# Performance work log

Hardware: AMD Instinct MI355X
Metric: run time of the kernel (lower is better)

The kernel has to match this reference:

```python
import jax, jax.numpy as jnp
import numpy as np

N_EXPERTS = 8
TOP_K = 2


def setup_inputs() -> dict:
    key = jax.random.key(0)
    k1, k2, k3, k4 = jax.random.split(key, 4)
    B, T, C, H, E = 2, 2048, 1024, 4096, N_EXPERTS
    x = jax.random.normal(k1, (B, T, C), dtype=jnp.float32)
    # weights scaled like standard init to keep activations well-behaved
    router_w = jax.random.normal(k2, (E, C), dtype=jnp.float32) * 0.02
    w1 = jax.random.normal(k3, (E, C, H), dtype=jnp.float32) * (1.0 / np.sqrt(C))
    w2 = jax.random.normal(k4, (E, H, C), dtype=jnp.float32) * (1.0 / np.sqrt(H))
    return {"x": x, "router_w": router_w, "w1": w1, "w2": w2}


def reference(x, router_w, w1, w2):
    B, T, C = x.shape
    E = N_EXPERTS
    xf = x.reshape(-1, C)                                   # [N, C], N = B*T
    logits = jnp.einsum('nc,ec->ne', xf, router_w)          # router (no bias)
    probs = jax.nn.softmax(logits, axis=-1)
    top_w, top_i = jax.lax.top_k(probs, TOP_K)              # [N, K]
    top_w = top_w / jnp.sum(top_w, axis=-1, keepdims=True)  # renormalize
    # combine weight per (token, expert): sum of top-k weights routed to e
    comb = jnp.einsum('nk,nke->ne', top_w, jax.nn.one_hot(top_i, E, dtype=xf.dtype))
    # dense all-expert compute (bias=False, exact GELU, dropout=0 at eval)
    h = jax.nn.gelu(jnp.einsum('nc,ech->enh', xf, w1), approximate=False)  # [E, N, H]
    y = jnp.einsum('enh,ehc->enc', h, w2)                   # [E, N, C]
    out = jnp.einsum('ne,enc->nc', comb, y)                 # weighted combine
    return out.reshape(B, T, C)
```

## Files before the change

kernel.cpp:

```cpp
#include <hip/hip_runtime.h>
#include <hip/hip_bf16.h>
#include <stdint.h>

#define NTOK 4096
#define CD   1024
#define HD   4096
#define NE   8

typedef __attribute__((ext_vector_type(8))) short bf16x8;
typedef __attribute__((ext_vector_type(4))) float f32x4;
typedef __attribute__((ext_vector_type(4))) unsigned short us4;

__device__ __forceinline__ unsigned short f2bf(float f){
  __hip_bfloat16 h = __float2bfloat16(f);
  return *reinterpret_cast<unsigned short*>(&h);
}

__global__ __launch_bounds__(256) void router_kernel(
    const float* __restrict__ x, const float* __restrict__ rw,
    unsigned short* __restrict__ x_bf, int* __restrict__ top_i,
    float* __restrict__ top_w, int* __restrict__ counts){
  __shared__ float rw_lds[NE*CD];
  int tid = threadIdx.x;
  for (int i = tid; i < NE*CD/4; i += 256)
    ((float4*)rw_lds)[i] = ((const float4*)rw)[i];
  __syncthreads();
  int l = tid & 63, w = tid >> 6;
  int n = blockIdx.x*4 + w;

  float4 xv[4];
  #pragma unroll
  for (int j = 0; j < 4; ++j)
    xv[j] = ((const float4*)(x + (size_t)n*CD))[l + j*64];

  #pragma unroll
  for (int j = 0; j < 4; ++j){
    us4 o; o.x = f2bf(xv[j].x); o.y = f2bf(xv[j].y); o.z = f2bf(xv[j].z); o.w = f2bf(xv[j].w);
    *(us4*)(x_bf + (size_t)n*CD + l*4 + j*256) = o;
  }

  double le[NE];
  #pragma unroll
  for (int e = 0; e < NE; ++e){
    double p = 0.0;
    #pragma unroll
    for (int j = 0; j < 4; ++j){
      float4 rv = ((const float4*)(rw_lds + e*CD))[l + j*64];
      p += (double)xv[j].x*rv.x + (double)xv[j].y*rv.y + (double)xv[j].z*rv.z + (double)xv[j].w*rv.w;
    }
    #pragma unroll
    for (int d = 32; d >= 1; d >>= 1) p += __shfl_xor(p, d);
    le[e] = p;
  }
  if (l == 0){
    double m = le[0];
    #pragma unroll
    for (int e = 1; e < NE; ++e) m = le[e] > m ? le[e] : m;
    double pe[NE], s = 0.0;
    #pragma unroll
    for (int e = 0; e < NE; ++e){ pe[e] = exp(le[e]-m); s += pe[e]; }
    (void)s;
    int i0 = 0;
    #pragma unroll
    for (int e = 1; e < NE; ++e) if (pe[e] > pe[i0]) i0 = e;
    int i1 = (i0 == 0) ? 1 : 0;
    #pragma unroll
    for (int e = 0; e < NE; ++e){ if (e == i0) continue; if (pe[e] > pe[i1]) i1 = e; }
    double w0 = pe[i0], w1v = pe[i1], wsum = w0 + w1v;
    top_i[2*n] = i0; top_i[2*n+1] = i1;
    top_w[2*n] = (float)(w0/wsum); top_w[2*n+1] = (float)(w1v/wsum);
    atomicAdd(&counts[i0], 1); atomicAdd(&counts[i1], 1);
  }
}

__global__ void scan_kernel(const int* __restrict__ counts, int* __restrict__ offsets, int* __restrict__ cursor){
  if (threadIdx.x == 0){
    int s = 0;
    for (int e = 0; e < NE; ++e){ offsets[e] = s; cursor[e] = s; s += counts[e]; }
  }
}

__global__ __launch_bounds__(256) void scatter_kernel(
    const int* __restrict__ top_i, const float* __restrict__ top_w,
    int* __restrict__ cursor, int* __restrict__ g_tok, float* __restrict__ g_w){
  int n = blockIdx.x*256 + threadIdx.x;
  #pragma unroll
  for (int k = 0; k < 2; ++k){
    int e = top_i[2*n+k];
    int pos = atomicAdd(&cursor[e], 1);
    g_tok[pos] = n;
    g_w[pos] = top_w[2*n+k];
  }
}

template<int R, int S>
__global__ __launch_bounds__(256) void transpose_cvt(const float* __restrict__ in, unsigned short* __restrict__ outp){
  __shared__ float tile[64][65];
  int e = blockIdx.z;
  const float* ip = in + (size_t)e*R*S;
  unsigned short* op = outp + (size_t)e*R*S;
  int s0 = blockIdx.x*64, r0 = blockIdx.y*64;
  int tid = threadIdx.x;
  #pragma unroll
  for (int i = 0; i < 4; ++i){
    int lin = i*256 + tid;
    int rr = lin >> 4, c4 = lin & 15;
    float4 v = *(const float4*)(ip + (size_t)(r0+rr)*S + s0 + c4*4);
    tile[rr][c4*4+0] = v.x; tile[rr][c4*4+1] = v.y;
    tile[rr][c4*4+2] = v.z; tile[rr][c4*4+3] = v.w;
  }
  __syncthreads();
  #pragma unroll
  for (int i = 0; i < 4; ++i){
    int lin = i*256 + tid;
    int ss = lin >> 4, rq = lin & 15;
    us4 o;
    o.x = f2bf(tile[rq*4+0][ss]);
    o.y = f2bf(tile[rq*4+1][ss]);
    o.z = f2bf(tile[rq*4+2][ss]);
    o.w = f2bf(tile[rq*4+3][ss]);
    *(us4*)(op + (size_t)(s0+ss)*R + r0 + rq*4) = o;
  }
}

template<int KDIM, int EPI>
__global__ __launch_bounds__(256, 2) void gemm2ph(
    const unsigned short* __restrict__ A_src,
    const unsigned short* __restrict__ B_src,
    unsigned short* __restrict__ h_out,
    float* __restrict__ outp,
    const int* __restrict__ g_tok,
    const float* __restrict__ g_w,
    const int* __restrict__ counts,
    const int* __restrict__ offsets,
    int NDIM){
  constexpr int NT = KDIM/64;
  __shared__ alignas(128) char lds[65536];

  int e = blockIdx.z;
  int n_e = counts[e];
  int m0 = blockIdx.y*128;
  if (m0 >= n_e) return;
  int n0 = blockIdx.x*128;
  int g_base = offsets[e];

  int tid = threadIdx.x, l = tid & 63, w = tid >> 6;
  int wr = w >> 1, wc = w & 1;
  int lrow = l & 15, q = l >> 4;

  const unsigned short* src[8];
  uint32_t dst[8];
  #pragma unroll
  for (int i = 0; i < 8; ++i){
    int s = w*8 + i;
    bool isA = s < 16;
    int srow = (s & 15)*8 + (l >> 3);
    int chunk = (l & 7) ^ (srow & 7);
    if (isA){
      int rg = m0 + srow; if (rg > n_e-1) rg = n_e-1;
      size_t arow;
      if (EPI == 0) arow = (size_t)g_tok[g_base + rg];
      else          arow = (size_t)(g_base + rg);
      src[i] = A_src + arow*(size_t)KDIM + chunk*8;
    } else {
      src[i] = B_src + ((size_t)e*NDIM + n0 + srow)*(size_t)KDIM + chunk*8;
    }
    dst[i] = (isA ? 0u : 16384u) + (uint32_t)(s & 15)*1024u;
  }

  uint32_t a_off[4], b_off[4];
  #pragma unroll
  for (int m = 0; m < 4; ++m){
    int ra = wr*64 + m*16 + lrow;
    a_off[m] = ra*128 + 16*(q ^ (ra & 7));
    int rb = wc*64 + m*16 + lrow;
    b_off[m] = 16384u + rb*128 + 16*(q ^ (rb & 7));
  }

  f32x4 acc[4][4] = {};

  #pragma unroll
  for (int i = 0; i < 8; ++i){
    __builtin_amdgcn_global_load_lds((const __attribute__((address_space(1))) void*)src[i],
                                     (__attribute__((address_space(3))) void*)&lds[dst[i]], 16, 0, 0);
    src[i] += 64;
  }
  __syncthreads();

  uint32_t buf = 0;
  for (int kt = 0; kt < NT; ++kt){
    if (kt + 1 < NT){
      uint32_t nb = (buf ^ 1)*32768u;
      #pragma unroll
      for (int i = 0; i < 8; ++i){
        __builtin_amdgcn_global_load_lds((const __attribute__((address_space(1))) void*)src[i],
                                         (__attribute__((address_space(3))) void*)&lds[dst[i] + nb], 16, 0, 0);
        src[i] += 64;
      }
    }
    uint32_t ro = buf*32768u;
    #pragma unroll
    for (int ks = 0; ks < 2; ++ks){
      bf16x8 av[4], bv[4];
      #pragma unroll
      for (int m = 0; m < 4; ++m){
        av[m] = *(const bf16x8*)&lds[(a_off[m] ^ (ks*64)) + ro];
        bv[m] = *(const bf16x8*)&lds[(b_off[m] ^ (ks*64)) + ro];
      }
      __builtin_amdgcn_s_setprio(1);
      #pragma unroll
      for (int m = 0; m < 4; ++m)
        #pragma unroll
        for (int n = 0; n < 4; ++n)
          acc[m][n] = __builtin_amdgcn_mfma_f32_16x16x32_bf16(av[m], bv[n], acc[m][n], 0, 0, 0);
      __builtin_amdgcn_s_setprio(0);
    }
    __syncthreads();
    buf ^= 1;
  }

  if (EPI == 0){
    #pragma unroll
    for (int m = 0; m < 4; ++m){
      #pragma unroll
      for (int j = 0; j < 4; ++j){
        int r = m0 + wr*64 + m*16 + q*4 + j;
        if (r < n_e){
          unsigned short* hp = h_out + (size_t)(g_base + r)*NDIM + n0 + wc*64 + lrow;
          #pragma unroll
          for (int n = 0; n < 4; ++n){
            float v = acc[m][n][j];
            v = 0.5f*v*(1.0f + erff(v*0.70710678118654752f));
            hp[n*16] = f2bf(v);
          }
        }
      }
    }
  } else {
    #pragma unroll
    for (int m = 0; m < 4; ++m){
      #pragma unroll
      for (int j = 0; j < 4; ++j){
        int r = m0 + wr*64 + m*16 + q*4 + j;
        if (r < n_e){
          int slot = g_base + r;
          int t = g_tok[slot];
          float wgt = g_w[slot];
          float* op = outp + (size_t)t*NDIM + n0 + wc*64 + lrow;
          #pragma unroll
          for (int n = 0; n < 4; ++n)
            atomicAdd(op + n*16, wgt*acc[m][n][j]);
        }
      }
    }
  }
}

extern "C" void kernel_launch(void* const* d_in, const int* in_sizes, int n_in,
                              void* d_out, int out_size, void* d_ws, size_t ws_size,
                              hipStream_t stream) {
  const float* x  = (const float*)d_in[0];
  const float* rw = (const float*)d_in[1];
  const float* w1 = (const float*)d_in[2];
  const float* w2 = (const float*)d_in[3];

  size_t off = 0;
  auto alloc = [&](size_t sz) -> char* {
    char* p = (char*)d_ws + off;
    off += (sz + 255) & ~(size_t)255;
    return p;
  };
  unsigned short* x_bf = (unsigned short*)alloc((size_t)NTOK*CD*2);
  unsigned short* w1t  = (unsigned short*)alloc((size_t)NE*CD*HD*2);
  unsigned short* w2t  = (unsigned short*)alloc((size_t)NE*CD*HD*2);
  unsigned short* hbuf = (unsigned short*)alloc((size_t)NTOK*2*HD*2);
  int*   top_i  = (int*)alloc(NTOK*2*4);
  float* top_w  = (float*)alloc(NTOK*2*4);
  int*   counts = (int*)alloc(64);
  int*   offs   = (int*)alloc(64);
  int*   cursor = (int*)alloc(64);
  int*   g_tok  = (int*)alloc(NTOK*2*4);
  float* g_w    = (float*)alloc(NTOK*2*4);
  (void)ws_size; (void)in_sizes; (void)n_in; (void)out_size;

  hipMemsetAsync(d_out, 0, (size_t)NTOK*CD*4, stream);
  hipMemsetAsync(counts, 0, 64, stream);

  router_kernel<<<dim3(NTOK/4), dim3(256), 0, stream>>>(x, rw, x_bf, top_i, top_w, counts);
  scan_kernel<<<dim3(1), dim3(64), 0, stream>>>(counts, offs, cursor);
  scatter_kernel<<<dim3(NTOK/256), dim3(256), 0, stream>>>(top_i, top_w, cursor, g_tok, g_w);

  transpose_cvt<CD, HD><<<dim3(HD/64, CD/64, NE), dim3(256), 0, stream>>>(w1, w1t);
  transpose_cvt<HD, CD><<<dim3(CD/64, HD/64, NE), dim3(256), 0, stream>>>(w2, w2t);

  gemm2ph<CD, 0><<<dim3(HD/128, 32, NE), dim3(256), 0, stream>>>(
      x_bf, w1t, hbuf, (float*)nullptr, g_tok, g_w, counts, offs, HD);
  gemm2ph<HD, 1><<<dim3(CD/128, 32, NE), dim3(256), 0, stream>>>(
      hbuf, w2t, (unsigned short*)nullptr, (float*)d_out, g_tok, g_w, counts, offs, CD);
}
```

Measured before the change: 484.7 us.

## Enlarge expert GEMM tiles to 256x256 with 512 threads and split-K second GEMM

Both grouped expert GEMMs move from 128x128 tiles with 4 waves to 256x256 tiles with 8 waves. Each wave now computes a 128x64 sub-tile, and the double-buffered LDS staging grows to 128KB. The goal is more MFMA work per byte loaded from global memory and from LDS. The down-projection GEMM also splits K=4096 into two halves along the z grid dimension, relying on the existing atomicAdd epilogue, so there are enough blocks once the tiles are larger. The risks are that large LDS use and higher register pressure limit residency to one block per CU, and that split-K doubles the number of atomics.

```diff
diff --git a/kernel.cpp b/kernel.cpp
--- a/kernel.cpp
+++ b/kernel.cpp
@@ -123,8 +123,8 @@
   }
 }
 
-template<int KDIM, int EPI>
-__global__ __launch_bounds__(256, 2) void gemm2ph(
+template<int KLEN, int SPLITK, int EPI>
+__global__ __launch_bounds__(512, 2) void gemm256(
     const unsigned short* __restrict__ A_src,
     const unsigned short* __restrict__ B_src,
     unsigned short* __restrict__ h_out,
@@ -133,51 +133,57 @@
     const float* __restrict__ g_w,
     const int* __restrict__ counts,
     const int* __restrict__ offsets,
-    int NDIM){
-  constexpr int NT = KDIM/64;
-  __shared__ alignas(128) char lds[65536];
-
-  int e = blockIdx.z;
+    int NDIM, int KSTRIDE){
+  constexpr int NT = KLEN/64;
+  __shared__ alignas(128) char lds[131072];
+
+  int z = blockIdx.z;
+  int e  = (SPLITK == 1) ? z : (z / SPLITK);
+  int kz = (SPLITK == 1) ? 0 : (z % SPLITK);
   int n_e = counts[e];
-  int m0 = blockIdx.y*128;
+  int m0 = blockIdx.y*256;
   if (m0 >= n_e) return;
-  int n0 = blockIdx.x*128;
+  int n0 = blockIdx.x*256;
   int g_base = offsets[e];
+  int kstart = kz*KLEN;
 
   int tid = threadIdx.x, l = tid & 63, w = tid >> 6;
-  int wr = w >> 1, wc = w & 1;
+  int wr = w >> 2, wc = w & 3;
   int lrow = l & 15, q = l >> 4;
 
   const unsigned short* src[8];
   uint32_t dst[8];
   #pragma unroll
   for (int i = 0; i < 8; ++i){
-    int s = w*8 + i;
-    bool isA = s < 16;
-    int srow = (s & 15)*8 + (l >> 3);
-    int chunk = (l & 7) ^ (srow & 7);
+    int s = w*4 + (i & 3);
+    bool isA = i < 4;
+    int row = s*8 + (l >> 3);
+    int chunk = (l & 7) ^ (row & 7);
     if (isA){
-      int rg = m0 + srow; if (rg > n_e-1) rg = n_e-1;
+      int rg = m0 + row; if (rg > n_e-1) rg = n_e-1;
       size_t arow;
       if (EPI == 0) arow = (size_t)g_tok[g_base + rg];
       else          arow = (size_t)(g_base + rg);
-      src[i] = A_src + arow*(size_t)KDIM + chunk*8;
+      src[i] = A_src + arow*(size_t)KSTRIDE + kstart + chunk*8;
     } else {
-      src[i] = B_src + ((size_t)e*NDIM + n0 + srow)*(size_t)KDIM + chunk*8;
-    }
-    dst[i] = (isA ? 0u : 16384u) + (uint32_t)(s & 15)*1024u;
-  }
-
-  uint32_t a_off[4], b_off[4];
-  #pragma unroll
-  for (int m = 0; m < 4; ++m){
-    int ra = wr*64 + m*16 + lrow;
+      src[i] = B_src + ((size_t)e*NDIM + n0 + row)*(size_t)KSTRIDE + kstart + chunk*8;
+    }
+    dst[i] = (isA ? 0u : 32768u) + (uint32_t)s*1024u;
+  }
+
+  uint32_t a_off[8], b_off[4];
+  #pragma unroll
+  for (int m = 0; m < 8; ++m){
+    int ra = wr*128 + m*16 + lrow;
     a_off[m] = ra*128 + 16*(q ^ (ra & 7));
-    int rb = wc*64 + m*16 + lrow;
-    b_off[m] = 16384u + rb*128 + 16*(q ^ (rb & 7));
-  }
-
-  f32x4 acc[4][4] = {};
+  }
+  #pragma unroll
+  for (int n = 0; n < 4; ++n){
+    int rb = wc*64 + n*16 + lrow;
+    b_off[n] = 32768u + rb*128 + 16*(q ^ (rb & 7));
+  }
+
+  f32x4 acc[8][4] = {};
 
   #pragma unroll
   for (int i = 0; i < 8; ++i){
@@ -190,7 +196,7 @@
   uint32_t buf = 0;
   for (int kt = 0; kt < NT; ++kt){
     if (kt + 1 < NT){
-      uint32_t nb = (buf ^ 1)*32768u;
+      uint32_t nb = (buf ^ 1)*65536u;
       #pragma unroll
       for (int i = 0; i < 8; ++i){
         __builtin_amdgcn_global_load_lds((const __attribute__((address_space(1))) void*)src[i],
@@ -198,18 +204,19 @@
         src[i] += 64;
       }
     }
-    uint32_t ro = buf*32768u;
+    uint32_t ro = buf*65536u;
     #pragma unroll
     for (int ks = 0; ks < 2; ++ks){
-      bf16x8 av[4], bv[4];
-      #pragma unroll
-      for (int m = 0; m < 4; ++m){
+      bf16x8 av[8], bv[4];
+      #pragma unroll
+      for (int m = 0; m < 8; ++m)
         av[m] = *(const bf16x8*)&lds[(a_off[m] ^ (ks*64)) + ro];
-        bv[m] = *(const bf16x8*)&lds[(b_off[m] ^ (ks*64)) + ro];
-      }
+      #pragma unroll
+      for (int n = 0; n < 4; ++n)
+        bv[n] = *(const bf16x8*)&lds[(b_off[n] ^ (ks*64)) + ro];
       __builtin_amdgcn_s_setprio(1);
       #pragma unroll
-      for (int m = 0; m < 4; ++m)
+      for (int m = 0; m < 8; ++m)
         #pragma unroll
         for (int n = 0; n < 4; ++n)
           acc[m][n] = __builtin_amdgcn_mfma_f32_16x16x32_bf16(av[m], bv[n], acc[m][n], 0, 0, 0);
@@ -221,10 +228,10 @@
 
   if (EPI == 0){
     #pragma unroll
-    for (int m = 0; m < 4; ++m){
+    for (int m = 0; m < 8; ++m){
       #pragma unroll
       for (int j = 0; j < 4; ++j){
-        int r = m0 + wr*64 + m*16 + q*4 + j;
+        int r = m0 + wr*128 + m*16 + q*4 + j;
         if (r < n_e){
           unsigned short* hp = h_out + (size_t)(g_base + r)*NDIM + n0 + wc*64 + lrow;
           #pragma unroll
@@ -238,10 +245,10 @@
     }
   } else {
     #pragma unroll
-    for (int m = 0; m < 4; ++m){
+    for (int m = 0; m < 8; ++m){
       #pragma unroll
       for (int j = 0; j < 4; ++j){
-        int r = m0 + wr*64 + m*16 + q*4 + j;
+        int r = m0 + wr*128 + m*16 + q*4 + j;
         if (r < n_e){
           int slot = g_base + r;
           int t = g_tok[slot];
@@ -293,8 +300,8 @@
   transpose_cvt<CD, HD><<<dim3(HD/64, CD/64, NE), dim3(256), 0, stream>>>(w1, w1t);
   transpose_cvt<HD, CD><<<dim3(CD/64, HD/64, NE), dim3(256), 0, stream>>>(w2, w2t);
 
-  gemm2ph<CD, 0><<<dim3(HD/128, 32, NE), dim3(256), 0, stream>>>(
-      x_bf, w1t, hbuf, (float*)nullptr, g_tok, g_w, counts, offs, HD);
-  gemm2ph<HD, 1><<<dim3(CD/128, 32, NE), dim3(256), 0, stream>>>(
-      hbuf, w2t, (unsigned short*)nullptr, (float*)d_out, g_tok, g_w, counts, offs, CD);
-}
+  gemm256<CD, 1, 0><<<dim3(HD/256, 8, NE), dim3(512), 0, stream>>>(
+      x_bf, w1t, hbuf, (float*)nullptr, g_tok, g_w, counts, offs, HD, CD);
+  gemm256<HD/2, 2, 1><<<dim3(CD/256, 8, NE*2), dim3(512), 0, stream>>>(
+      hbuf, w2t, (unsigned short*)nullptr, (float*)d_out, g_tok, g_w, counts, offs, CD, HD);
+}
```

New measurement: 509.3 us. +5.1%, slower.

## Make expert GEMMs persistent with balanced tile scheduling and split-K

Applied to the files above, without the earlier changes.

Replaces the per-expert 3D grid, which launches many early-exiting blocks for empty m-tiles, with a persistent 512-block launch. Each block walks a contiguous range of flattened (expert, m-tile, n-tile, k-chunk) work items and flushes its accumulator whenever the output tile changes. The second GEMM is split into four 1024-wide K chunks that each atomically add into the output, raising parallelism for the small N=1024 dimension. In exchange, the down-projection now does more atomic traffic, and tiles that straddle block boundaries become partial sums that need extra flushes.

```diff
diff --git a/kernel.cpp b/kernel.cpp
--- a/kernel.cpp
+++ b/kernel.cpp
@@ -123,8 +123,8 @@
   }
 }
 
-template<int KDIM, int EPI>
-__global__ __launch_bounds__(256, 2) void gemm2ph(
+template<int GN, int KCH, int EPI>
+__global__ __launch_bounds__(256, 2) void gemm_pers(
     const unsigned short* __restrict__ A_src,
     const unsigned short* __restrict__ B_src,
     unsigned short* __restrict__ h_out,
@@ -133,40 +133,25 @@
     const float* __restrict__ g_w,
     const int* __restrict__ counts,
     const int* __restrict__ offsets,
-    int NDIM){
-  constexpr int NT = KDIM/64;
+    int NDIM, int KSTRIDE, int NBLK){
   __shared__ alignas(128) char lds[65536];
 
-  int e = blockIdx.z;
-  int n_e = counts[e];
-  int m0 = blockIdx.y*128;
-  if (m0 >= n_e) return;
-  int n0 = blockIdx.x*128;
-  int g_base = offsets[e];
+  int ne_[NE], cum[NE+1];
+  cum[0] = 0;
+  #pragma unroll
+  for (int e = 0; e < NE; ++e){
+    ne_[e] = counts[e];
+    int mt = (ne_[e] + 127) >> 7;
+    cum[e+1] = cum[e] + mt*GN*KCH;
+  }
+  int T = cum[NE];
+  int bid = blockIdx.x;
+  int t0 = (int)(((long long)T * bid) / NBLK);
+  int t1 = (int)(((long long)T * (bid+1)) / NBLK);
 
   int tid = threadIdx.x, l = tid & 63, w = tid >> 6;
   int wr = w >> 1, wc = w & 1;
   int lrow = l & 15, q = l >> 4;
-
-  const unsigned short* src[8];
-  uint32_t dst[8];
-  #pragma unroll
-  for (int i = 0; i < 8; ++i){
-    int s = w*8 + i;
-    bool isA = s < 16;
-    int srow = (s & 15)*8 + (l >> 3);
-    int chunk = (l & 7) ^ (srow & 7);
-    if (isA){
-      int rg = m0 + srow; if (rg > n_e-1) rg = n_e-1;
-      size_t arow;
-      if (EPI == 0) arow = (size_t)g_tok[g_base + rg];
-      else          arow = (size_t)(g_base + rg);
-      src[i] = A_src + arow*(size_t)KDIM + chunk*8;
-    } else {
-      src[i] = B_src + ((size_t)e*NDIM + n0 + srow)*(size_t)KDIM + chunk*8;
-    }
-    dst[i] = (isA ? 0u : 16384u) + (uint32_t)(s & 15)*1024u;
-  }
 
   uint32_t a_off[4], b_off[4];
   #pragma unroll
@@ -177,83 +162,132 @@
     b_off[m] = 16384u + rb*128 + 16*(q ^ (rb & 7));
   }
 
-  f32x4 acc[4][4] = {};
-
-  #pragma unroll
-  for (int i = 0; i < 8; ++i){
-    __builtin_amdgcn_global_load_lds((const __attribute__((address_space(1))) void*)src[i],
-                                     (__attribute__((address_space(3))) void*)&lds[dst[i]], 16, 0, 0);
-    src[i] += 64;
-  }
-  __syncthreads();
-
-  uint32_t buf = 0;
-  for (int kt = 0; kt < NT; ++kt){
-    if (kt + 1 < NT){
-      uint32_t nb = (buf ^ 1)*32768u;
-      #pragma unroll
-      for (int i = 0; i < 8; ++i){
-        __builtin_amdgcn_global_load_lds((const __attribute__((address_space(1))) void*)src[i],
-                                         (__attribute__((address_space(3))) void*)&lds[dst[i] + nb], 16, 0, 0);
-        src[i] += 64;
-      }
-    }
-    uint32_t ro = buf*32768u;
-    #pragma unroll
-    for (int ks = 0; ks < 2; ++ks){
-      bf16x8 av[4], bv[4];
-      #pragma unroll
-      for (int m = 0; m < 4; ++m){
-        av[m] = *(const bf16x8*)&lds[(a_off[m] ^ (ks*64)) + ro];
-        bv[m] = *(const bf16x8*)&lds[(b_off[m] ^ (ks*64)) + ro];
-      }
-      __builtin_amdgcn_s_setprio(1);
+  f32x4 acc[4][4];
+  int cur_key = -1, fe = 0, fmi = 0, fni = 0;
+
+  auto flush = [&](){
+    int n_e = ne_[fe], g_base = offsets[fe];
+    int m0 = fmi*128, n0 = fni*128;
+    if (EPI == 0){
       #pragma unroll
       for (int m = 0; m < 4; ++m)
         #pragma unroll
-        for (int n = 0; n < 4; ++n)
-          acc[m][n] = __builtin_amdgcn_mfma_f32_16x16x32_bf16(av[m], bv[n], acc[m][n], 0, 0, 0);
-      __builtin_amdgcn_s_setprio(0);
-    }
-    __syncthreads();
-    buf ^= 1;
-  }
-
-  if (EPI == 0){
-    #pragma unroll
-    for (int m = 0; m < 4; ++m){
-      #pragma unroll
-      for (int j = 0; j < 4; ++j){
-        int r = m0 + wr*64 + m*16 + q*4 + j;
-        if (r < n_e){
-          unsigned short* hp = h_out + (size_t)(g_base + r)*NDIM + n0 + wc*64 + lrow;
-          #pragma unroll
-          for (int n = 0; n < 4; ++n){
-            float v = acc[m][n][j];
-            v = 0.5f*v*(1.0f + erff(v*0.70710678118654752f));
-            hp[n*16] = f2bf(v);
+        for (int j = 0; j < 4; ++j){
+          int r = m0 + wr*64 + m*16 + q*4 + j;
+          if (r < n_e){
+            unsigned short* hp = h_out + (size_t)(g_base + r)*NDIM + n0 + wc*64 + lrow;
+            #pragma unroll
+            for (int n = 0; n < 4; ++n){
+              float v = acc[m][n][j];
+              v = 0.5f*v*(1.0f + erff(v*0.70710678118654752f));
+              hp[n*16] = f2bf(v);
+            }
           }
         }
+    } else {
+      #pragma unroll
+      for (int m = 0; m < 4; ++m)
+        #pragma unroll
+        for (int j = 0; j < 4; ++j){
+          int r = m0 + wr*64 + m*16 + q*4 + j;
+          if (r < n_e){
+            int slot = g_base + r;
+            int t_ = g_tok[slot];
+            float wgt = g_w[slot];
+            float* op = outp + (size_t)t_*NDIM + n0 + wc*64 + lrow;
+            #pragma unroll
+            for (int n = 0; n < 4; ++n)
+              atomicAdd(op + n*16, wgt*acc[m][n][j]);
+          }
+        }
+    }
+  };
+
+  for (int t = t0; t < t1; ++t){
+    int e = 0;
+    #pragma unroll
+    for (int ee = 1; ee < NE; ++ee) if (t >= cum[ee]) e = ee;
+    int rem = t - cum[e];
+    int kc = rem % KCH;
+    int ni = (rem / KCH) % GN;
+    int mi = rem / (KCH*GN);
+    int key = t / KCH;
+
+    if (key != cur_key){
+      if (cur_key >= 0) flush();
+      #pragma unroll
+      for (int m = 0; m < 4; ++m)
+        #pragma unroll
+        for (int n = 0; n < 4; ++n)
+          acc[m][n] = f32x4{0.f,0.f,0.f,0.f};
+      cur_key = key; fe = e; fmi = mi; fni = ni;
+    }
+
+    int n_e = ne_[e], g_base = offsets[e];
+    int m0 = mi*128, n0 = ni*128, kstart = kc*1024;
+
+    const unsigned short* src[8];
+    uint32_t dst[8];
+    #pragma unroll
+    for (int i = 0; i < 8; ++i){
+      int s = w*8 + i;
+      bool isA = s < 16;
+      int srow = (s & 15)*8 + (l >> 3);
+      int chunk = (l & 7) ^ (srow & 7);
+      if (isA){
+        int rg = m0 + srow; if (rg > n_e-1) rg = n_e-1;
+        size_t arow;
+        if (EPI == 0) arow = (size_t)g_tok[g_base + rg];
+        else          arow = (size_t)(g_base + rg);
+        src[i] = A_src + arow*(size_t)KSTRIDE + kstart + chunk*8;
+      } else {
+        src[i] = B_src + ((size_t)e*NDIM + n0 + srow)*(size_t)KSTRIDE + kstart + chunk*8;
       }
-    }
-  } else {
-    #pragma unroll
-    for (int m = 0; m < 4; ++m){
+      dst[i] = (isA ? 0u : 16384u) + (uint32_t)(s & 15)*1024u;
+    }
+
+    #pragma unroll
+    for (int i = 0; i < 8; ++i){
+      __builtin_amdgcn_global_load_lds((const __attribute__((address_space(1))) void*)src[i],
+                                       (__attribute__((address_space(3))) void*)&lds[dst[i]], 16, 0, 0);
+      src[i] += 64;
+    }
+    __syncthreads();
+
+    uint32_t buf = 0;
+    #pragma unroll 1
+    for (int kt = 0; kt < 16; ++kt){
+      if (kt + 1 < 16){
+        uint32_t nb = (buf ^ 1)*32768u;
+        #pragma unroll
+        for (int i = 0; i < 8; ++i){
+          __builtin_amdgcn_global_load_lds((const __attribute__((address_space(1))) void*)src[i],
+                                           (__attribute__((address_space(3))) void*)&lds[dst[i] + nb], 16, 0, 0);
+          src[i] += 64;
+        }
+      }
+      uint32_t ro = buf*32768u;
       #pragma unroll
-      for (int j = 0; j < 4; ++j){
-        int r = m0 + wr*64 + m*16 + q*4 + j;
-        if (r < n_e){
-          int slot = g_base + r;
-          int t = g_tok[slot];
-          float wgt = g_w[slot];
-          float* op = outp + (size_t)t*NDIM + n0 + wc*64 + lrow;
+      for (int ks = 0; ks < 2; ++ks){
+        bf16x8 av[4], bv[4];
+        #pragma unroll
+        for (int m = 0; m < 4; ++m){
+          av[m] = *(const bf16x8*)&lds[(a_off[m] ^ (ks*64)) + ro];
+          bv[m] = *(const bf16x8*)&lds[(b_off[m] ^ (ks*64)) + ro];
+        }
+        __builtin_amdgcn_s_setprio(1);
+        #pragma unroll
+        for (int m = 0; m < 4; ++m)
           #pragma unroll
           for (int n = 0; n < 4; ++n)
-            atomicAdd(op + n*16, wgt*acc[m][n][j]);
-        }
+            acc[m][n] = __builtin_amdgcn_mfma_f32_16x16x32_bf16(av[m], bv[n], acc[m][n], 0, 0, 0);
+        __builtin_amdgcn_s_setprio(0);
       }
-    }
-  }
+      __syncthreads();
+      buf ^= 1;
+    }
+  }
+  if (cur_key >= 0) flush();
 }
 
 extern "C" void kernel_launch(void* const* d_in, const int* in_sizes, int n_in,
@@ -293,8 +327,8 @@
   transpose_cvt<CD, HD><<<dim3(HD/64, CD/64, NE), dim3(256), 0, stream>>>(w1, w1t);
   transpose_cvt<HD, CD><<<dim3(CD/64, HD/64, NE), dim3(256), 0, stream>>>(w2, w2t);
 
-  gemm2ph<CD, 0><<<dim3(HD/128, 32, NE), dim3(256), 0, stream>>>(
-      x_bf, w1t, hbuf, (float*)nullptr, g_tok, g_w, counts, offs, HD);
-  gemm2ph<HD, 1><<<dim3(CD/128, 32, NE), dim3(256), 0, stream>>>(
-      hbuf, w2t, (unsigned short*)nullptr, (float*)d_out, g_tok, g_w, counts, offs, CD);
-}
+  gemm_pers<32, 1, 0><<<dim3(512), dim3(256), 0, stream>>>(
+      x_bf, w1t, hbuf, (float*)nullptr, g_tok, g_w, counts, offs, HD, CD, 512);
+  gemm_pers<8, 4, 1><<<dim3(512), dim3(256), 0, stream>>>(
+      hbuf, w2t, (unsigned short*)nullptr, (float*)d_out, g_tok, g_w, counts, offs, CD, HD, 512);
+}
```

Measured after the change: 579.7 us. +19.6%, slower.
